# Kernel optimization log

Hardware: AMD Instinct MI355X
Metric: run time of the kernel (lower is better)

## Reference

```python
import jax, jax.numpy as jnp
import numpy as np

EPS = 1e-8  # torch cosine_similarity eps


def setup_inputs() -> dict:
    key = jax.random.key(0)
    ks = jax.random.split(key, 6)
    N, D, E, mask_dim = 50000, 128, 600000, 1
    x = jax.random.normal(ks[0], (N, D), dtype=jnp.float32)
    mask = jax.random.normal(ks[1], (N, mask_dim), dtype=jnp.float32)
    edge_index = jax.random.randint(ks[2], (2, E), 0, N, dtype=jnp.int64)
    # Linear(input_dim, input_dim) params (orthogonal-ish init not needed for math check)
    W = jax.random.normal(ks[3], (D, D), dtype=jnp.float32) / np.sqrt(D)
    b_lin = jax.random.normal(ks[4], (D,), dtype=jnp.float32) * 0.01
    alpha = jnp.float32(0.001)
    bias = jnp.ones((mask_dim,), dtype=jnp.float32) * -3.0
    return {"x": x, "mask": mask, "edge_index": edge_index,
            "W": W, "b_lin": b_lin, "alpha": alpha, "bias": bias}


def _forward(x, mask, W, b_lin, alpha, bias, edge_index, K=5):
    N = x.shape[0]
    # x_fn: Linear + Tanh
    h = jnp.tanh(x @ W.T + b_lin)                    # [N, D]
    row, col = edge_index[0], edge_index[1]
    hs, hd = h[row], h[col]                          # [E, D] gathers
    ns = jnp.maximum(jnp.linalg.norm(hs, axis=-1), EPS)
    nd = jnp.maximum(jnp.linalg.norm(hd, axis=-1), EPS)
    cos = jnp.sum(hs * hd, axis=-1) / (ns * nd)      # [E]
    edge_weights = jax.nn.relu(cos)

    # APPNP with PyG defaults: gcn_norm with self-loops (weight 1), sym norm
    loops = jnp.arange(N, dtype=row.dtype)
    r2 = jnp.concatenate([row, loops])
    c2 = jnp.concatenate([col, loops])
    w2 = jnp.concatenate([edge_weights, jnp.ones((N,), dtype=edge_weights.dtype)])
    deg = jax.ops.segment_sum(w2, c2, num_segments=N)
    dinv = jnp.where(deg > 0, deg ** -0.5, 0.0)
    norm = dinv[r2] * w2 * dinv[c2]                  # [E+N]

    h0 = jax.nn.relu(mask)                           # [N, 1]
    f = h0
    for _ in range(K):
        msg = norm[:, None] * f[r2]                  # gather + weight
        agg = jax.ops.segment_sum(msg, c2, num_segments=N)  # scatter-add to targets
        f = (1.0 - alpha) * agg + alpha * h0
    fill = jnp.tanh(f - jax.nn.softplus(bias))
    return fill, edge_weights


def reference(x, mask, edge_index, W, b_lin, alpha, bias):
    return _forward(x, mask, W, b_lin, alpha, bias, edge_index, K=5)
```

## Files before the change

### kernel.cpp

```cpp
#include <hip/hip_runtime.h>
#include <hip/hip_bf16.h>
#include <hip/hip_fp16.h>
#include <math.h>

typedef _Float16 half8 __attribute__((ext_vector_type(8)));
typedef float f32x4 __attribute__((ext_vector_type(4)));

__device__ __forceinline__ float tanh_fast(float v) {
  float e = __expf(v + v);
  return 1.0f - 2.0f * __builtin_amdgcn_rcpf(e + 1.0f);
}

__device__ __forceinline__ float dot8h(float4 a, float4 b) {
  const __half2* pa = (const __half2*)&a;
  const __half2* pb = (const __half2*)&b;
  float s = 0.0f;
#pragma unroll
  for (int i = 0; i < 4; ++i) {
    float2 fa = __half22float2(pa[i]);
    float2 fb = __half22float2(pb[i]);
    s = fmaf(fa.x, fb.x, s);
    s = fmaf(fa.y, fb.y, s);
  }
  return s;
}

__global__ __launch_bounds__(256) void k_front(
    const float* __restrict__ x, const float* __restrict__ W,
    const float* __restrict__ bl, const float* __restrict__ mask,
    const int* __restrict__ cols, __half* __restrict__ hn,
    int* __restrict__ cnt8, unsigned short* __restrict__ rank,
    float* __restrict__ h0, float* __restrict__ f_a, int N, int E, int nblk) {
  __shared__ _Float16 wsh[128 * 128];
  const int tid = threadIdx.x;
  const int bid = blockIdx.x;

  for (int i = tid; i < 2048; i += 256) {
    int row = i >> 4, cc = i & 15;
    const float4* wr = (const float4*)(W + row * 128 + cc * 8);
    float4 a = wr[0], b = wr[1];
    half8 h;
    h[0] = (_Float16)a.x; h[1] = (_Float16)a.y;
    h[2] = (_Float16)a.z; h[3] = (_Float16)a.w;
    h[4] = (_Float16)b.x; h[5] = (_Float16)b.y;
    h[6] = (_Float16)b.z; h[7] = (_Float16)b.w;
    *(half8*)((char*)wsh + row * 256 + ((cc * 16) ^ ((row & 7) << 4))) = h;
  }
  __syncthreads();

  const int wv = tid >> 6, lane = tid & 63;
  const int row0 = bid * 64 + wv * 16;
  if (row0 < N) {
    const int r = lane & 15;
    const int g = lane >> 4;
    half8 afrag[4];
    {
      const float4* xr = (const float4*)(x + (size_t)(row0 + r) * 128);
#pragma unroll
      for (int ks = 0; ks < 4; ++ks) {
        float4 lo = xr[ks * 8 + g * 2];
        float4 hi = xr[ks * 8 + g * 2 + 1];
        half8 a;
        a[0] = (_Float16)lo.x; a[1] = (_Float16)lo.y;
        a[2] = (_Float16)lo.z; a[3] = (_Float16)lo.w;
        a[4] = (_Float16)hi.x; a[5] = (_Float16)hi.y;
        a[6] = (_Float16)hi.z; a[7] = (_Float16)hi.w;
        afrag[ks] = a;
      }
    }
    f32x4 acc[8];
#pragma unroll
    for (int c = 0; c < 8; ++c) acc[c] = (f32x4){0.f, 0.f, 0.f, 0.f};
#pragma unroll
    for (int c = 0; c < 8; ++c) {
      const char* base = (const char*)wsh + (c * 16 + r) * 256;
      const int sw = ((c * 16 + r) & 7) << 4;
#pragma unroll
      for (int ks = 0; ks < 4; ++ks) {
        half8 b = *(const half8*)(base + ((ks * 64 + g * 16) ^ sw));
        acc[c] = __builtin_amdgcn_mfma_f32_16x16x32_f16(afrag[ks], b, acc[c],
                                                        0, 0, 0);
      }
    }
    float t[8][4];
    float ss[4] = {0.f, 0.f, 0.f, 0.f};
#pragma unroll
    for (int c = 0; c < 8; ++c) {
      float bv = bl[c * 16 + r];
#pragma unroll
      for (int j = 0; j < 4; ++j) {
        float tv = tanh_fast(acc[c][j] + bv);
        t[c][j] = tv;
        ss[j] = fmaf(tv, tv, ss[j]);
      }
    }
#pragma unroll
    for (int j = 0; j < 4; ++j) {
#pragma unroll
      for (int o = 8; o; o >>= 1) ss[j] += __shfl_xor(ss[j], o);
      ss[j] = 1.0f / fmaxf(sqrtf(ss[j]), 1e-8f);
    }
#pragma unroll
    for (int c = 0; c < 8; ++c)
#pragma unroll
      for (int j = 0; j < 4; ++j)
        hn[(size_t)(row0 + g * 4 + j) * 128 + c * 16 + r] =
            __float2half_rn(t[c][j] * ss[j]);
  }

  const int tg = bid * 256 + tid;
  const int NT = nblk * 256;
  for (int i = tg; i < N; i += NT) {
    float v = fmaxf(mask[i], 0.0f);
    h0[i] = v;
    f_a[i] = v;
  }
  for (int e = tg; e < E; e += NT) {
    int c = cols[e];
    int copy = (e >> 8) & 7;
    int rk = atomicAdd(cnt8 + copy * N + c, 1);
    rank[e] = (unsigned short)rk;
  }
}

__global__ __launch_bounds__(256) void k_scan_a(const int* __restrict__ cnt8,
                                                int* __restrict__ bsum,
                                                int N) {
  __shared__ int s[256];
  int i = blockIdx.x * 256 + threadIdx.x;
  int tot = 0;
  if (i < N) {
#pragma unroll
    for (int j = 0; j < 8; ++j) tot += cnt8[j * N + i];
  }
  s[threadIdx.x] = tot;
  __syncthreads();
  for (int d = 128; d; d >>= 1) {
    if (threadIdx.x < d) s[threadIdx.x] += s[threadIdx.x + d];
    __syncthreads();
  }
  if (threadIdx.x == 0) bsum[blockIdx.x] = s[0];
}

__global__ __launch_bounds__(256) void k_scan_bc(int* __restrict__ cnt8,
                                                 const int* __restrict__ bsum,
                                                 int* __restrict__ off, int N,
                                                 int E, int NCH) {
  __shared__ int bscan[2 * 256];
  __shared__ int cscan[2 * 256];
  const int t = threadIdx.x, bid = blockIdx.x;
  int bv = (t < NCH) ? bsum[t] : 0;
  bscan[t] = bv;
  __syncthreads();
  int a = 0;
  for (int d = 1; d < 256; d <<= 1) {
    int v2 = bscan[a * 256 + t];
    if (t >= d) v2 += bscan[a * 256 + t - d];
    bscan[(a ^ 1) * 256 + t] = v2;
    __syncthreads();
    a ^= 1;
  }
  int bpre = (bid > 0) ? bscan[a * 256 + bid - 1] : 0;
  int i = bid * 256 + t;
  int cj[8];
  int tot = 0;
  if (i < N) {
#pragma unroll
    for (int j = 0; j < 8; ++j) {
      cj[j] = cnt8[j * N + i];
      tot += cj[j];
    }
  }
  cscan[t] = tot;
  __syncthreads();
  int b2 = 0;
  for (int d = 1; d < 256; d <<= 1) {
    int v2 = cscan[b2 * 256 + t];
    if (t >= d) v2 += cscan[b2 * 256 + t - d];
    cscan[(b2 ^ 1) * 256 + t] = v2;
    __syncthreads();
    b2 ^= 1;
  }
  if (i < N) {
    int excl = cscan[b2 * 256 + t] - tot + bpre;
    off[i] = excl;
    int run = excl;
#pragma unroll
    for (int j = 0; j < 8; ++j) {
      cnt8[j * N + i] = run;
      run += cj[j];
    }
  }
  if (bid == 0 && t == 0) off[N] = E;
}

__global__ void k_build(const int* __restrict__ rows,
                        const int* __restrict__ cols,
                        const int* __restrict__ base8,
                        const unsigned short* __restrict__ rank,
                        unsigned* __restrict__ rec, int* __restrict__ perm,
                        int N, int E) {
  int e = blockIdx.x * 256 + threadIdx.x;
  if (e >= E) return;
  unsigned r = (unsigned)rows[e], c = (unsigned)cols[e];
  int copy = (e >> 8) & 7;
  int pos = base8[copy * N + (int)c] + (int)rank[e];
  rec[pos] = r | (c << 16);
  perm[e] = pos;
}

__global__ __launch_bounds__(256) void k_edge_cos(
    const __half* __restrict__ hn, const unsigned* __restrict__ rec,
    float* __restrict__ csr_w, unsigned short* __restrict__ src16, int E,
    int Q) {
  int t = blockIdx.x * 256 + threadIdx.x;
  int q = t >> 2, sub = t & 3;
  if (q >= Q) return;
  const int p0 = q, p1 = q + Q;
  const bool has1 = p1 < E;
  unsigned rc0 = rec[p0];
  unsigned rc1 = has1 ? rec[p1] : rc0;
  const float4* hr0 = (const float4*)(hn + (size_t)(rc0 & 0xffffu) * 128);
  const float4* hr1 = (const float4*)(hn + (size_t)(rc1 & 0xffffu) * 128);
  float4 r00 = hr0[sub], r01 = hr0[sub + 4], r02 = hr0[sub + 8],
         r03 = hr0[sub + 12];
  float4 r10 = hr1[sub], r11 = hr1[sub + 4], r12 = hr1[sub + 8],
         r13 = hr1[sub + 12];
  const float4* hc0 = (const float4*)(hn + (size_t)(rc0 >> 16) * 128);
  const float4* hc1 = (const float4*)(hn + (size_t)(rc1 >> 16) * 128);
  float d0 = dot8h(r00, hc0[sub]) + dot8h(r01, hc0[sub + 4]) +
             dot8h(r02, hc0[sub + 8]) + dot8h(r03, hc0[sub + 12]);
  float d1 = dot8h(r10, hc1[sub]) + dot8h(r11, hc1[sub + 4]) +
             dot8h(r12, hc1[sub + 8]) + dot8h(r13, hc1[sub + 12]);
  d0 += __shfl_xor(d0, 1);
  d0 += __shfl_xor(d0, 2);
  d1 += __shfl_xor(d1, 1);
  d1 += __shfl_xor(d1, 2);
  if (sub == 0) {
    csr_w[p0] = fmaxf(d0, 0.0f);
    src16[p0] = (unsigned short)(rc0 & 0xffffu);
    if (has1) {
      csr_w[p1] = fmaxf(d1, 0.0f);
      src16[p1] = (unsigned short)(rc1 & 0xffffu);
    }
  }
}

__global__ __launch_bounds__(256) void k_unperm_rsd(
    const float* __restrict__ csr_w, const int* __restrict__ perm,
    const int* __restrict__ off, float* __restrict__ ew,
    float* __restrict__ rsd, int N, int E) {
  int t = blockIdx.x * 256 + threadIdx.x;
  if (t < E) ew[t] = csr_w[perm[t]];
  int n = t >> 2, sub = t & 3;
  if (n < N) {
    int s0 = off[n], s1 = off[n + 1];
    float s = 0.0f;
    for (int i = s0 + sub; i < s1; i += 4) s += csr_w[i];
    s += __shfl_xor(s, 1);
    s += __shfl_xor(s, 2);
    if (sub == 0) rsd[n] = rsqrtf(1.0f + s);
  }
}

__global__ __launch_bounds__(256) void k_prop(
    const float* __restrict__ f_in, float* __restrict__ f_out,
    float* __restrict__ csr_w, const unsigned short* __restrict__ src16,
    const int* __restrict__ off, const float* __restrict__ h0,
    const float* __restrict__ rsd, const float* __restrict__ alpha_p,
    const float* __restrict__ bias_p, float* __restrict__ fill, int N,
    int mode) {
  int t = blockIdx.x * 256 + threadIdx.x;
  int n = t >> 2, sub = t & 3;
  if (n >= N) return;
  float rs_n = rsd[n];
  int s0 = off[n], s1 = off[n + 1];
  float part = 0.0f;
  if (mode & 1) {
    for (int i = s0 + sub; i < s1; i += 4) {
      int s = src16[i];
      float wn = csr_w[i] * rs_n * rsd[s];
      csr_w[i] = wn;
      part = fmaf(wn, f_in[s], part);
    }
  } else {
    for (int i = s0 + sub; i < s1; i += 4)
      part = fmaf(csr_w[i], f_in[src16[i]], part);
  }
  part += __shfl_xor(part, 1);
  part += __shfl_xor(part, 2);
  if (sub == 0) {
    float a = alpha_p[0];
    float agg = part + f_in[n] * rs_n * rs_n;
    float fn = (1.0f - a) * agg + a * h0[n];
    if (mode & 2) {
      float b = bias_p[0];
      float sp = (b > 20.0f) ? b : log1pf(expf(b));
      fill[n] = tanhf(fn - sp);
    } else {
      f_out[n] = fn;
    }
  }
}

extern "C" void kernel_launch(void* const* d_in, const int* in_sizes, int n_in,
                              void* d_out, int out_size, void* d_ws,
                              size_t ws_size, hipStream_t stream) {
  const float* x = (const float*)d_in[0];
  const float* mask = (const float*)d_in[1];
  const int* ei = (const int*)d_in[2];
  const float* W = (const float*)d_in[3];
  const float* bl = (const float*)d_in[4];
  const float* alpha = (const float*)d_in[5];
  const float* bias = (const float*)d_in[6];

  const int D = 128;
  const int N = in_sizes[0] / D;
  const int E = in_sizes[2] / 2;
  const int* rows = ei;
  const int* cols = ei + E;

  float* fill = (float*)d_out;
  float* ew = (float*)d_out + N;

  char* w = (char*)d_ws;
  size_t off_b = 0;
  auto alloc = [&](size_t bytes) -> void* {
    void* p = (void*)(w + off_b);
    off_b = (off_b + bytes + 255) & ~(size_t)255;
    return p;
  };
  __half* hn = (__half*)alloc((size_t)N * D * sizeof(__half));
  int* cnt8 = (int*)alloc((size_t)8 * N * sizeof(int));
  unsigned short* rank =
      (unsigned short*)alloc((size_t)E * sizeof(unsigned short));
  int* off = (int*)alloc((size_t)(N + 1) * sizeof(int));
  int* bsum = (int*)alloc(256 * sizeof(int));
  unsigned* rec = (unsigned*)alloc((size_t)E * sizeof(unsigned));
  int* perm = (int*)alloc((size_t)E * sizeof(int));
  float* csr_w = (float*)alloc((size_t)E * sizeof(float));
  unsigned short* src16 =
      (unsigned short*)alloc((size_t)E * sizeof(unsigned short));
  float* h0 = (float*)alloc((size_t)N * sizeof(float));
  float* f_a = (float*)alloc((size_t)N * sizeof(float));
  float* f_b = (float*)alloc((size_t)N * sizeof(float));
  float* rsd = (float*)alloc((size_t)N * sizeof(float));
  (void)ws_size;

  const int NCH = (N + 255) / 256;
  const int nb_E = (E + 255) / 256;
  const int FRONT_BLOCKS = (N + 63) / 64;

  hipMemsetAsync(cnt8, 0, (size_t)8 * N * sizeof(int), stream);
  k_front<<<FRONT_BLOCKS, 256, 0, stream>>>(x, W, bl, mask, cols, hn, cnt8,
                                            rank, h0, f_a, N, E, FRONT_BLOCKS);
  k_scan_a<<<NCH, 256, 0, stream>>>(cnt8, bsum, N);
  k_scan_bc<<<NCH, 256, 0, stream>>>(cnt8, bsum, off, N, E, NCH);
  k_build<<<nb_E, 256, 0, stream>>>(rows, cols, cnt8, rank, rec, perm, N, E);
  const int Q = (E + 1) / 2;
  k_edge_cos<<<(Q * 4 + 255) / 256, 256, 0, stream>>>(hn, rec, csr_w, src16,
                                                      E, Q);
  k_unperm_rsd<<<nb_E, 256, 0, stream>>>(csr_w, perm, off, ew, rsd, N, E);
  const float* fi = f_a;
  float* fo = f_b;
  for (int it = 0; it < 5; ++it) {
    int mode = (it == 0 ? 1 : 0) | (it == 4 ? 2 : 0);
    k_prop<<<(N * 4 + 255) / 256, 256, 0, stream>>>(
        fi, fo, csr_w, src16, off, h0, rsd, alpha, bias, fill, N, mode);
    const float* tmp = fo;
    fo = (float*)fi;
    fi = tmp;
  }
}
```

Measured before the change: 120.6 us.

## Halve front blocks, process two row tiles per wave with x prefetch

The front kernel now launches half as many blocks, and each wave handles two 16-row tiles in a grid-strided loop. The x rows for the first tile are loaded before the W staging, so that load overlaps the weight conversion into LDS. The next tile's x is prefetched while the current tile's MFMAs run. The per-block cost of staging W into LDS is paid over twice as many rows. The cost is more register pressure from the prefetch buffers and fewer blocks, which lowers parallelism. The first x load now has no bounds check, which works because N is a multiple of 16.

```diff
diff --git a/kernel.cpp b/kernel.cpp
--- a/kernel.cpp
+++ b/kernel.cpp
@@ -30,42 +30,77 @@
     const float* __restrict__ bl, const float* __restrict__ mask,
     const int* __restrict__ cols, __half* __restrict__ hn,
     int* __restrict__ cnt8, unsigned short* __restrict__ rank,
-    float* __restrict__ h0, float* __restrict__ f_a, int N, int E, int nblk) {
+    float* __restrict__ h0, float* __restrict__ f_a, int N, int E, int nblk,
+    int wstride, int ntiles) {
   __shared__ _Float16 wsh[128 * 128];
   const int tid = threadIdx.x;
   const int bid = blockIdx.x;
-
-  for (int i = tid; i < 2048; i += 256) {
-    int row = i >> 4, cc = i & 15;
-    const float4* wr = (const float4*)(W + row * 128 + cc * 8);
-    float4 a = wr[0], b = wr[1];
-    half8 h;
-    h[0] = (_Float16)a.x; h[1] = (_Float16)a.y;
-    h[2] = (_Float16)a.z; h[3] = (_Float16)a.w;
-    h[4] = (_Float16)b.x; h[5] = (_Float16)b.y;
-    h[6] = (_Float16)b.z; h[7] = (_Float16)b.w;
-    *(half8*)((char*)wsh + row * 256 + ((cc * 16) ^ ((row & 7) << 4))) = h;
+  const int wv = tid >> 6, lane = tid & 63;
+  const int r = lane & 15;
+  const int g = lane >> 4;
+
+  int t0 = bid * 4 + wv;
+
+  float4 xv[8];
+  {
+    const float4* xr = (const float4*)(x + (size_t)(t0 * 16 + r) * 128);
+#pragma unroll
+    for (int ks = 0; ks < 4; ++ks) {
+      xv[ks * 2] = xr[ks * 8 + g * 2];
+      xv[ks * 2 + 1] = xr[ks * 8 + g * 2 + 1];
+    }
+  }
+
+  {
+    float4 wa[8], wb[8];
+#pragma unroll
+    for (int k = 0; k < 8; ++k) {
+      int i = tid + k * 256;
+      const float4* wr = (const float4*)(W + (i >> 4) * 128 + (i & 15) * 8);
+      wa[k] = wr[0];
+      wb[k] = wr[1];
+    }
+#pragma unroll
+    for (int k = 0; k < 8; ++k) {
+      int i = tid + k * 256;
+      int row = i >> 4, cc = i & 15;
+      half8 h;
+      h[0] = (_Float16)wa[k].x; h[1] = (_Float16)wa[k].y;
+      h[2] = (_Float16)wa[k].z; h[3] = (_Float16)wa[k].w;
+      h[4] = (_Float16)wb[k].x; h[5] = (_Float16)wb[k].y;
+      h[6] = (_Float16)wb[k].z; h[7] = (_Float16)wb[k].w;
+      *(half8*)((char*)wsh + row * 256 + ((cc * 16) ^ ((row & 7) << 4))) = h;
+    }
   }
   __syncthreads();
 
-  const int wv = tid >> 6, lane = tid & 63;
-  const int row0 = bid * 64 + wv * 16;
-  if (row0 < N) {
-    const int r = lane & 15;
-    const int g = lane >> 4;
+  float bv[8];
+#pragma unroll
+  for (int c = 0; c < 8; ++c) bv[c] = bl[c * 16 + r];
+
+  int t = t0;
+#pragma unroll
+  for (int it = 0; it < 2; ++it) {
+    const int row0 = t * 16;
     half8 afrag[4];
-    {
-      const float4* xr = (const float4*)(x + (size_t)(row0 + r) * 128);
+#pragma unroll
+    for (int ks = 0; ks < 4; ++ks) {
+      float4 lo = xv[ks * 2], hi = xv[ks * 2 + 1];
+      half8 a;
+      a[0] = (_Float16)lo.x; a[1] = (_Float16)lo.y;
+      a[2] = (_Float16)lo.z; a[3] = (_Float16)lo.w;
+      a[4] = (_Float16)hi.x; a[5] = (_Float16)hi.y;
+      a[6] = (_Float16)hi.z; a[7] = (_Float16)hi.w;
+      afrag[ks] = a;
+    }
+    const int tn = t + wstride;
+    const bool hasnext = (it == 0) && (tn < ntiles);
+    if (hasnext) {
+      const float4* xr = (const float4*)(x + (size_t)(tn * 16 + r) * 128);
 #pragma unroll
       for (int ks = 0; ks < 4; ++ks) {
-        float4 lo = xr[ks * 8 + g * 2];
-        float4 hi = xr[ks * 8 + g * 2 + 1];
-        half8 a;
-        a[0] = (_Float16)lo.x; a[1] = (_Float16)lo.y;
-        a[2] = (_Float16)lo.z; a[3] = (_Float16)lo.w;
-        a[4] = (_Float16)hi.x; a[5] = (_Float16)hi.y;
-        a[6] = (_Float16)hi.z; a[7] = (_Float16)hi.w;
-        afrag[ks] = a;
+        xv[ks * 2] = xr[ks * 8 + g * 2];
+        xv[ks * 2 + 1] = xr[ks * 8 + g * 2 + 1];
       }
     }
     f32x4 acc[8];
@@ -82,15 +117,14 @@
                                                         0, 0, 0);
       }
     }
-    float t[8][4];
+    float tt[8][4];
     float ss[4] = {0.f, 0.f, 0.f, 0.f};
 #pragma unroll
     for (int c = 0; c < 8; ++c) {
-      float bv = bl[c * 16 + r];
 #pragma unroll
       for (int j = 0; j < 4; ++j) {
-        float tv = tanh_fast(acc[c][j] + bv);
-        t[c][j] = tv;
+        float tv = tanh_fast(acc[c][j] + bv[c]);
+        tt[c][j] = tv;
         ss[j] = fmaf(tv, tv, ss[j]);
       }
     }
@@ -105,7 +139,9 @@
 #pragma unroll
       for (int j = 0; j < 4; ++j)
         hn[(size_t)(row0 + g * 4 + j) * 128 + c * 16 + r] =
-            __float2half_rn(t[c][j] * ss[j]);
+            __float2half_rn(tt[c][j] * ss[j]);
+    if (!hasnext) break;
+    t = tn;
   }
 
   const int tg = bid * 256 + tid;
@@ -349,11 +385,14 @@
 
   const int NCH = (N + 255) / 256;
   const int nb_E = (E + 255) / 256;
-  const int FRONT_BLOCKS = (N + 63) / 64;
+  const int NTILES = (N + 15) / 16;
+  const int FRONT_BLOCKS = (NTILES + 7) / 8;
+  const int WSTRIDE = FRONT_BLOCKS * 4;
 
   hipMemsetAsync(cnt8, 0, (size_t)8 * N * sizeof(int), stream);
   k_front<<<FRONT_BLOCKS, 256, 0, stream>>>(x, W, bl, mask, cols, hn, cnt8,
-                                            rank, h0, f_a, N, E, FRONT_BLOCKS);
+                                            rank, h0, f_a, N, E, FRONT_BLOCKS,
+                                            WSTRIDE, NTILES);
   k_scan_a<<<NCH, 256, 0, stream>>>(cnt8, bsum, N);
   k_scan_bc<<<NCH, 256, 0, stream>>>(cnt8, bsum, off, N, E, NCH);
   k_build<<<nb_E, 256, 0, stream>>>(rows, cols, cnt8, rank, rec, perm, N, E);
```

After: 118.4 us. Within noise of the previous version (-1.8%).
